# Optimization experiments

Hardware: AMD Instinct MI355X
Metric: run time of the kernel (lower is better)

## Reference

```python
import jax, jax.numpy as jnp
import numpy as np

B, N, F_IN = 8, 4096, 32
NRP = 1024
D_MODEL = 512
K = 64  # max_num_neighbors
STAGE_CFG = ((1024, 0.05), (256, 0.3), (64, 0.5))  # (num_samples=ceil(0.25*N_in), radius)


def fps(pos, m):
    """Farthest point sampling of m points from pos (N,3), deterministic start at 0."""
    d = jnp.sum((pos - pos[0]) ** 2, axis=-1)
    idxs = jnp.zeros((m,), jnp.int32)
    def body(i, carry):
        idxs, d = carry
        nxt = jnp.argmax(d).astype(jnp.int32)
        d = jnp.minimum(d, jnp.sum((pos - pos[nxt]) ** 2, axis=-1))
        return (idxs.at[i].set(nxt), d)
    idxs, _ = jax.lax.fori_loop(1, m, body, (idxs, d))
    return idxs


def apply_mlp(h, ws, bs):
    for w, b in zip(ws[:-1], bs[:-1]):
        h = jax.nn.relu(h @ w + b)
    return h @ ws[-1] + bs[-1]


def sa_stage(x, pos, m, r, ws, bs):
    """SAModule: FPS -> radius neighbors (<=K) -> PointNetConv (gather, MLP, max-scatter)."""
    idx = jax.vmap(lambda p: fps(p, m))(pos)                          # (B,m)
    pos_s = jnp.take_along_axis(pos, idx[..., None], axis=1)          # (B,m,3)
    d2 = jnp.sum((pos_s[:, :, None, :] - pos[:, None, :, :]) ** 2, -1)  # (B,m,N)
    neg = jnp.where(d2 <= r * r, -d2, -jnp.inf)
    vals, nbr = jax.lax.top_k(neg, K)                                 # (B,m,K) nearest within r
    valid = vals > -jnp.inf                                           # self always valid (d2=0)
    x_j = jax.vmap(lambda xb, nb: xb[nb])(x, nbr)                     # (B,m,K,F) gather
    p_j = jax.vmap(lambda pb, nb: pb[nb])(pos, nbr)                   # (B,m,K,3)
    h = jnp.concatenate([x_j, p_j - pos_s[:, :, None, :]], axis=-1)   # message input
    h = apply_mlp(h, ws, bs)
    h = jnp.where(valid[..., None], h, -jnp.inf)
    return jnp.max(h, axis=2), pos_s                                  # max aggregation


def _forward(point_cloud_features, point_cloud, emb_table, point_id_emb, stage_params):
    x = emb_table[point_cloud_features[..., 0]]                       # (B,N,F_IN)
    x = x.at[:, :NRP].add(point_id_emb)
    pos = point_cloud
    for (m, r), (ws, bs) in zip(STAGE_CFG, stage_params):
        x, pos = sa_stage(x, pos, m, r, ws, bs)
    return x, pos                                                     # (B,64,D_MODEL), (B,64,3)


def setup_inputs() -> dict:
    key = jax.random.key(0)
    ks = iter(jax.random.split(key, 64))
    def nrm(shape, s=0.05):
        return s * jax.random.normal(next(ks), shape, dtype=jnp.float32)
    inp = {
        "point_cloud_features": jax.random.randint(next(ks), (B, N, 1), 0, 3),
        "point_cloud": jax.random.uniform(next(ks), (B, N, 3), dtype=jnp.float32),
        "emb_table": nrm((3, F_IN), 1.0),
        "point_id_emb": nrm((1, NRP, F_IN), 1.0),
    }
    dims = {"s1": [3 + F_IN, 64, 64, 64], "s2": [64 + 3, 128, 128, 256], "s3": [256 + 3, 256, 512, D_MODEL]}
    for s, d in dims.items():
        for i in range(3):
            inp[f"{s}w{i}"] = nrm((d[i], d[i + 1]))
            inp[f"{s}b{i}"] = jnp.zeros((d[i + 1],), jnp.float32)
    return inp


def reference(point_cloud_features, point_cloud, emb_table, point_id_emb,
              s1w0, s1b0, s1w1, s1b1, s1w2, s1b2,
              s2w0, s2b0, s2w1, s2b1, s2w2, s2b2,
              s3w0, s3b0, s3w1, s3b1, s3w2, s3b2):
    stage_params = [
        ([s1w0, s1w1, s1w2], [s1b0, s1b1, s1b2]),
        ([s2w0, s2w1, s2w2], [s2b0, s2b1, s2b2]),
        ([s3w0, s3w1, s3w2], [s3b0, s3b1, s3b2]),
    ]
    return _forward(point_cloud_features, point_cloud, emb_table, point_id_emb, stage_params)
```

## Files before the change

### kernel.cpp

```cpp
#include <hip/hip_runtime.h>

#define DEVI static __device__ __forceinline__

constexpr int B = 8;
constexpr int N0 = 4096;
constexpr int KNB = 64;

typedef float f32x2 __attribute__((ext_vector_type(2)));

DEVI float dist2f(float ax, float ay, float az, float bx, float by, float bz) {
#pragma clang fp contract(off)
  float dx = ax - bx;
  float dy = ay - by;
  float dz = az - bz;
  return (dx * dx + dy * dy) + dz * dz;
}
DEVI f32x2 dist2v(f32x2 ax, f32x2 ay, f32x2 az, float bx, float by, float bz) {
#pragma clang fp contract(off)
  f32x2 dx = ax - bx;
  f32x2 dy = ay - by;
  f32x2 dz = az - bz;
  return (dx * dx + dy * dy) + dz * dz;
}

DEVI unsigned long long packMinKey(float v, int i) {
  return ((unsigned long long)__float_as_uint(v) << 32) | (unsigned int)i;
}

template <int CTRL, int RM>
DEVI float dppMaxF32(float v) {
  int o = __builtin_amdgcn_update_dpp(__float_as_int(v), __float_as_int(v),
                                      CTRL, RM, 0xf, false);
  return fmaxf(v, __int_as_float(o));
}
DEVI float waveMaxF32(float v) {
  v = dppMaxF32<0x111, 0xf>(v);
  v = dppMaxF32<0x112, 0xf>(v);
  v = dppMaxF32<0x114, 0xf>(v);
  v = dppMaxF32<0x118, 0xf>(v);
  v = dppMaxF32<0x142, 0xa>(v);
  v = dppMaxF32<0x143, 0xc>(v);
  return __int_as_float(__builtin_amdgcn_readlane(__float_as_int(v), 63));
}
template <int CTRL, int RM>
DEVI unsigned dppMinU32(unsigned v) {
  int o = __builtin_amdgcn_update_dpp((int)v, (int)v, CTRL, RM, 0xf, false);
  unsigned ov = (unsigned)o;
  return v < ov ? v : ov;
}
DEVI unsigned waveMinU32(unsigned v) {
  v = dppMinU32<0x111, 0xf>(v);
  v = dppMinU32<0x112, 0xf>(v);
  v = dppMinU32<0x114, 0xf>(v);
  v = dppMinU32<0x118, 0xf>(v);
  v = dppMinU32<0x142, 0xa>(v);
  v = dppMinU32<0x143, 0xc>(v);
  return (unsigned)__builtin_amdgcn_readlane((int)v, 63);
}

__global__ void __launch_bounds__(256) x0_kernel(const int* __restrict__ feat,
                                                 const float* __restrict__ emb,
                                                 const float* __restrict__ pid,
                                                 float* __restrict__ x0) {
  int gid = blockIdx.x * 256 + threadIdx.x;
  if (gid >= B * N0 * 32) return;
  int c = gid & 31;
  int bn = gid >> 5;
  int n = bn & (N0 - 1);
  int f = feat[bn];
  float v = emb[f * 32 + c];
  if (n < 1024) v += pid[n * 32 + c];
  x0[gid] = v;
}

template <int NPTS, int M, int BLK>
__global__ void __launch_bounds__(BLK) fps_kernel(const float* __restrict__ pos,
                                                  float* __restrict__ pos_out) {
  constexpr int EPT = NPTS / BLK;
  constexpr int EP2 = EPT / 2;
  constexpr int NW = BLK / 64;
  __shared__ float4 posl[NPTS];
  __shared__ float4 outp[M];
  __shared__ alignas(16) unsigned long long redk[2][NW < 2 ? 2 : NW];
  const int b = blockIdx.x;
  const int t = threadIdx.x;
  const float* pb = pos + (size_t)b * NPTS * 3;
  f32x2 px[EP2], py[EP2], pz[EP2], d[EP2];
#pragma unroll
  for (int e = 0; e < EP2; ++e) {
    int i0 = t + (2 * e) * BLK;
    int i1 = t + (2 * e + 1) * BLK;
    float x0 = pb[i0 * 3 + 0], y0 = pb[i0 * 3 + 1], z0 = pb[i0 * 3 + 2];
    float x1 = pb[i1 * 3 + 0], y1 = pb[i1 * 3 + 1], z1 = pb[i1 * 3 + 2];
    px[e] = (f32x2){x0, x1};
    py[e] = (f32x2){y0, y1};
    pz[e] = (f32x2){z0, z1};
    posl[i0] = make_float4(x0, y0, z0, 0.f);
    posl[i1] = make_float4(x1, y1, z1, 0.f);
  }
  float sx = pb[0], sy = pb[1], sz = pb[2];
  if (t == 0) outp[0] = make_float4(sx, sy, sz, 0.f);
#pragma unroll
  for (int e = 0; e < EP2; ++e) d[e] = dist2v(px[e], py[e], pz[e], sx, sy, sz);

  for (int it = 1; it < M; ++it) {
    float lm = fmaxf(d[0].x, d[0].y);
#pragma unroll
    for (int e = 1; e < EP2; ++e) lm = fmaxf(lm, fmaxf(d[e].x, d[e].y));
    const float vstar = waveMaxF32(lm);
    unsigned cand = 0xffffffffu;
#pragma unroll
    for (int e = 0; e < EP2; ++e) {
      unsigned c0 = (d[e].x == vstar) ? (unsigned)(t + (2 * e) * BLK) : 0xffffffffu;
      unsigned c1 = (d[e].y == vstar) ? (unsigned)(t + (2 * e + 1) * BLK) : 0xffffffffu;
      cand = cand < c0 ? cand : c0;
      cand = cand < c1 ? cand : c1;
    }
    cand = waveMinU32(cand);
    unsigned sel;
    if constexpr (NW > 1) {
      if ((t & 63) == 0) {
        unsigned long long key =
            ((unsigned long long)__float_as_uint(vstar) << 32) |
            (unsigned)(0x7fffffffu - cand);
        redk[it & 1][t >> 6] = key;
      }
      __syncthreads();
      unsigned long long kk = redk[it & 1][0];
#pragma unroll
      for (int w = 1; w < NW; ++w) {
        unsigned long long o = redk[it & 1][w];
        kk = (kk > o) ? kk : o;
      }
      sel = 0x7fffffffu - (unsigned)(kk & 0xffffffffULL);
    } else {
      sel = cand;
    }
    float4 sp = posl[sel];
    if (t == 0) outp[it] = sp;
#pragma unroll
    for (int e = 0; e < EP2; ++e) {
      f32x2 nd = dist2v(px[e], py[e], pz[e], sp.x, sp.y, sp.z);
      d[e].x = fminf(d[e].x, nd.x);
      d[e].y = fminf(d[e].y, nd.y);
    }
  }
  __syncthreads();
  for (int m = t; m < M; m += BLK) {
    float4 q = outp[m];
    pos_out[(size_t)(b * M + m) * 3 + 0] = q.x;
    pos_out[(size_t)(b * M + m) * 3 + 1] = q.y;
    pos_out[(size_t)(b * M + m) * 3 + 2] = q.z;
  }
}

template <int NPTS, int M>
__global__ void __launch_bounds__(256) radius_kernel(const float* __restrict__ pos,
                                                     const float* __restrict__ pos_s,
                                                     float r2,
                                                     int* __restrict__ nbr,
                                                     int* __restrict__ cnt) {
  __shared__ unsigned long long candkey[NPTS];
  __shared__ int ctr;
  const int blk = blockIdx.x;
  const int t = threadIdx.x;
  const int b = blk / M;
  const float* pb = pos + (size_t)b * NPTS * 3;
  const float cx = pos_s[(size_t)blk * 3 + 0];
  const float cy = pos_s[(size_t)blk * 3 + 1];
  const float cz = pos_s[(size_t)blk * 3 + 2];
  if (t == 0) ctr = 0;
  __syncthreads();
  for (int j = t; j < NPTS; j += 256) {
    float d2 = dist2f(pb[j * 3 + 0], pb[j * 3 + 1], pb[j * 3 + 2], cx, cy, cz);
    if (d2 <= r2) {
      int p = atomicAdd(&ctr, 1);
      candkey[p] = packMinKey(d2, j);
      if (p < KNB) nbr[(size_t)blk * KNB + p] = j;
    }
  }
  __syncthreads();
  const int c = ctr;
  if (c <= KNB) {
    if (t == 0) cnt[blk] = c;
    return;
  }
  for (int s = t; s < c; s += 256) {
    unsigned long long mykey = candkey[s];
    int rank = 0;
#pragma unroll 4
    for (int j = 0; j < c; ++j) {
      rank += (candkey[j] < mykey) ? 1 : 0;
    }
    if (rank < KNB)
      nbr[(size_t)blk * KNB + rank] = (int)(unsigned)(mykey & 0xffffffffULL);
  }
  if (t == 0) cnt[blk] = KNB;
}

__global__ void __launch_bounds__(64) conv1_kernel(
    const float* __restrict__ x0, const float* __restrict__ pos,
    const float* __restrict__ pos_s, const int* __restrict__ nbr,
    const int* __restrict__ cntp,
    const float* __restrict__ w0, const float* __restrict__ b0,
    const float* __restrict__ w1, const float* __restrict__ b1,
    const float* __restrict__ w2, const float* __restrict__ b2,
    float* __restrict__ x1) {
  __shared__ float ins[35];
  __shared__ float h[64];
  const int blk = blockIdx.x;
  const int t = threadIdx.x;
  const int b = blk >> 10;
  const int c = cntp[blk];
  const float cx = pos_s[(size_t)blk * 3 + 0];
  const float cy = pos_s[(size_t)blk * 3 + 1];
  const float cz = pos_s[(size_t)blk * 3 + 2];
  float best = -__builtin_inff();
  for (int r = 0; r < c; ++r) {
    int j = nbr[(size_t)blk * KNB + r];
    if (t < 32) {
      ins[t] = x0[((size_t)(b * N0) + j) * 32 + t];
    } else if (t < 35) {
      float pv = pos[((size_t)(b * N0) + j) * 3 + (t - 32)];
      float cv = (t == 32) ? cx : (t == 33) ? cy : cz;
      ins[t] = pv - cv;
    }
    __syncthreads();
    float v = b0[t];
#pragma unroll
    for (int i = 0; i < 35; ++i) v = fmaf(ins[i], w0[i * 64 + t], v);
    v = fmaxf(v, 0.f);
    h[t] = v;
    __syncthreads();
    float v2 = b1[t];
#pragma unroll
    for (int i = 0; i < 64; ++i) v2 = fmaf(h[i], w1[i * 64 + t], v2);
    v2 = fmaxf(v2, 0.f);
    __syncthreads();
    h[t] = v2;
    __syncthreads();
    float v3 = b2[t];
#pragma unroll
    for (int i = 0; i < 64; ++i) v3 = fmaf(h[i], w2[i * 64 + t], v3);
    best = fmaxf(best, v3);
    __syncthreads();
  }
  x1[(size_t)blk * 64 + t] = best;
}

__global__ void __launch_bounds__(256) conv2_kernel(
    const float* __restrict__ x1, const float* __restrict__ pos1,
    const float* __restrict__ pos2, const int* __restrict__ nbr,
    const int* __restrict__ cntp,
    const float* __restrict__ w0, const float* __restrict__ b0,
    const float* __restrict__ w1, const float* __restrict__ b1,
    const float* __restrict__ w2, const float* __restrict__ b2,
    float* __restrict__ x2) {
  __shared__ __attribute__((aligned(16))) float msg[64][68];
  __shared__ __attribute__((aligned(16))) float h[64][128];
  __shared__ float red[8][256];
  const int blk = blockIdx.x;
  const int t = threadIdx.x;
  const int b = blk >> 8;
  const int c = cntp[blk];
  const float cx = pos2[(size_t)blk * 3 + 0];
  const float cy = pos2[(size_t)blk * 3 + 1];
  const float cz = pos2[(size_t)blk * 3 + 2];
  for (int idx = t; idx < 64 * 68; idx += 256) {
    int r = idx / 68;
    int k = idx - r * 68;
    float v = 0.f;
    if (r < c && k < 67) {
      int j = nbr[(size_t)blk * KNB + r];
      if (k < 64) {
        v = x1[((size_t)(b * 1024) + j) * 64 + k];
      } else {
        float pv = pos1[((size_t)(b * 1024) + j) * 3 + (k - 64)];
        v = pv - ((k == 64) ? cx : (k == 65) ? cy : cz);
      }
    }
    msg[r][k] = v;
  }
  __syncthreads();
  const int rg = t >> 5;
  const int cg = t & 31;
  {
    float acc[8][4] = {};
    for (int i4 = 0; i4 < 16; ++i4) {
      float wv[4][4];
#pragma unroll
      for (int k = 0; k < 4; ++k) {
        float4 q = *(const float4*)&w0[(size_t)(i4 * 4 + k) * 128 + cg * 4];
        wv[k][0] = q.x; wv[k][1] = q.y; wv[k][2] = q.z; wv[k][3] = q.w;
      }
#pragma unroll
      for (int rr = 0; rr < 8; ++rr) {
        float4 aq = *(const float4*)&msg[rg * 8 + rr][i4 * 4];
        float a[4] = {aq.x, aq.y, aq.z, aq.w};
#pragma unroll
        for (int k = 0; k < 4; ++k)
#pragma unroll
          for (int cc = 0; cc < 4; ++cc)
            acc[rr][cc] = fmaf(a[k], wv[k][cc], acc[rr][cc]);
      }
    }
#pragma unroll
    for (int i = 64; i < 67; ++i) {
      float wv[4];
#pragma unroll
      for (int cc = 0; cc < 4; ++cc) wv[cc] = w0[(size_t)i * 128 + cg * 4 + cc];
#pragma unroll
      for (int rr = 0; rr < 8; ++rr) {
        float a = msg[rg * 8 + rr][i];
#pragma unroll
        for (int cc = 0; cc < 4; ++cc) acc[rr][cc] = fmaf(a, wv[cc], acc[rr][cc]);
      }
    }
#pragma unroll
    for (int rr = 0; rr < 8; ++rr)
#pragma unroll
      for (int cc = 0; cc < 4; ++cc)
        h[rg * 8 + rr][cg * 4 + cc] = fmaxf(acc[rr][cc] + b0[cg * 4 + cc], 0.f);
  }
  __syncthreads();
  {
    float acc[8][4] = {};
    for (int i4 = 0; i4 < 32; ++i4) {
      float wv[4][4];
#pragma unroll
      for (int k = 0; k < 4; ++k) {
        float4 q = *(const float4*)&w1[(size_t)(i4 * 4 + k) * 128 + cg * 4];
        wv[k][0] = q.x; wv[k][1] = q.y; wv[k][2] = q.z; wv[k][3] = q.w;
      }
#pragma unroll
      for (int rr = 0; rr < 8; ++rr) {
        float4 aq = *(const float4*)&h[rg * 8 + rr][i4 * 4];
        float a[4] = {aq.x, aq.y, aq.z, aq.w};
#pragma unroll
        for (int k = 0; k < 4; ++k)
#pragma unroll
          for (int cc = 0; cc < 4; ++cc)
            acc[rr][cc] = fmaf(a[k], wv[k][cc], acc[rr][cc]);
      }
    }
    __syncthreads();
#pragma unroll
    for (int rr = 0; rr < 8; ++rr)
#pragma unroll
      for (int cc = 0; cc < 4; ++cc)
        h[rg * 8 + rr][cg * 4 + cc] = fmaxf(acc[rr][cc] + b1[cg * 4 + cc], 0.f);
  }
  __syncthreads();
  {
    float acc[8][8] = {};
    for (int i4 = 0; i4 < 32; ++i4) {
      float wv[4][8];
#pragma unroll
      for (int k = 0; k < 4; ++k) {
        float4 q0 = *(const float4*)&w2[(size_t)(i4 * 4 + k) * 256 + cg * 8];
        float4 q1 = *(const float4*)&w2[(size_t)(i4 * 4 + k) * 256 + cg * 8 + 4];
        wv[k][0] = q0.x; wv[k][1] = q0.y; wv[k][2] = q0.z; wv[k][3] = q0.w;
        wv[k][4] = q1.x; wv[k][5] = q1.y; wv[k][6] = q1.z; wv[k][7] = q1.w;
      }
#pragma unroll
      for (int rr = 0; rr < 8; ++rr) {
        float4 aq = *(const float4*)&h[rg * 8 + rr][i4 * 4];
        float a[4] = {aq.x, aq.y, aq.z, aq.w};
#pragma unroll
        for (int k = 0; k < 4; ++k)
#pragma unroll
          for (int cc = 0; cc < 8; ++cc)
            acc[rr][cc] = fmaf(a[k], wv[k][cc], acc[rr][cc]);
      }
    }
    float mx[8];
#pragma unroll
    for (int cc = 0; cc < 8; ++cc) mx[cc] = -__builtin_inff();
#pragma unroll
    for (int rr = 0; rr < 8; ++rr) {
      if (rg * 8 + rr < c) {
#pragma unroll
        for (int cc = 0; cc < 8; ++cc)
          mx[cc] = fmaxf(mx[cc], acc[rr][cc] + b2[cg * 8 + cc]);
      }
    }
#pragma unroll
    for (int cc = 0; cc < 8; ++cc) red[rg][cg * 8 + cc] = mx[cc];
  }
  __syncthreads();
  {
    float v = red[0][t];
#pragma unroll
    for (int g = 1; g < 8; ++g) v = fmaxf(v, red[g][t]);
    x2[(size_t)blk * 256 + t] = v;
  }
}

__global__ void __launch_bounds__(256) conv3_kernel(
    const float* __restrict__ x2, const float* __restrict__ pos2,
    const float* __restrict__ pos3, const int* __restrict__ nbr,
    const int* __restrict__ cntp,
    const float* __restrict__ w0, const float* __restrict__ b0,
    const float* __restrict__ w1, const float* __restrict__ b1,
    const float* __restrict__ w2, const float* __restrict__ b2,
    float* __restrict__ out) {
  __shared__ __attribute__((aligned(16))) float msg[16][260];
  __shared__ __attribute__((aligned(16))) float h[16][512];
  __shared__ float red[4][512];
  __shared__ float omax[512];
  const int blk = blockIdx.x;
  const int t = threadIdx.x;
  const int b = blk >> 6;
  const int c = cntp[blk];
  const float cx = pos3[(size_t)blk * 3 + 0];
  const float cy = pos3[(size_t)blk * 3 + 1];
  const float cz = pos3[(size_t)blk * 3 + 2];
  omax[t] = -__builtin_inff();
  omax[t + 256] = -__builtin_inff();
  const int rg = t >> 6;
  const int cg = t & 63;
  __syncthreads();
  for (int ch = 0; ch < 4; ++ch) {
    if (ch * 16 >= c) break;
    for (int idx = t; idx < 16 * 260; idx += 256) {
      int r = idx / 260;
      int k = idx - r * 260;
      int rglob = ch * 16 + r;
      float v = 0.f;
      if (rglob < c && k < 259) {
        int j = nbr[(size_t)blk * KNB + rglob];
        if (k < 256) {
          v = x2[((size_t)(b * 256) + j) * 256 + k];
        } else {
          float pv = pos2[((size_t)(b * 256) + j) * 3 + (k - 256)];
          v = pv - ((k == 256) ? cx : (k == 257) ? cy : cz);
        }
      }
      msg[r][k] = v;
    }
    __syncthreads();
    {
      float acc[4][4] = {};
      for (int i4 = 0; i4 < 64; ++i4) {
        float wv[4][4];
#pragma unroll
        for (int k = 0; k < 4; ++k) {
          float4 q = *(const float4*)&w0[(size_t)(i4 * 4 + k) * 256 + cg * 4];
          wv[k][0] = q.x; wv[k][1] = q.y; wv[k][2] = q.z; wv[k][3] = q.w;
        }
#pragma unroll
        for (int rr = 0; rr < 4; ++rr) {
          float4 aq = *(const float4*)&msg[rg * 4 + rr][i4 * 4];
          float a[4] = {aq.x, aq.y, aq.z, aq.w};
#pragma unroll
          for (int k = 0; k < 4; ++k)
#pragma unroll
            for (int cc = 0; cc < 4; ++cc)
              acc[rr][cc] = fmaf(a[k], wv[k][cc], acc[rr][cc]);
        }
      }
#pragma unroll
      for (int i = 256; i < 259; ++i) {
        float wv[4];
#pragma unroll
        for (int cc = 0; cc < 4; ++cc) wv[cc] = w0[(size_t)i * 256 + cg * 4 + cc];
#pragma unroll
        for (int rr = 0; rr < 4; ++rr) {
          float a = msg[rg * 4 + rr][i];
#pragma unroll
          for (int cc = 0; cc < 4; ++cc) acc[rr][cc] = fmaf(a, wv[cc], acc[rr][cc]);
        }
      }
#pragma unroll
      for (int rr = 0; rr < 4; ++rr)
#pragma unroll
        for (int cc = 0; cc < 4; ++cc)
          h[rg * 4 + rr][cg * 4 + cc] = fmaxf(acc[rr][cc] + b0[cg * 4 + cc], 0.f);
    }
    __syncthreads();
    {
      float acc[4][8] = {};
      for (int i4 = 0; i4 < 64; ++i4) {
        float wv[4][8];
#pragma unroll
        for (int k = 0; k < 4; ++k) {
          float4 q0 = *(const float4*)&w1[(size_t)(i4 * 4 + k) * 512 + cg * 8];
          float4 q1 = *(const float4*)&w1[(size_t)(i4 * 4 + k) * 512 + cg * 8 + 4];
          wv[k][0] = q0.x; wv[k][1] = q0.y; wv[k][2] = q0.z; wv[k][3] = q0.w;
          wv[k][4] = q1.x; wv[k][5] = q1.y; wv[k][6] = q1.z; wv[k][7] = q1.w;
        }
#pragma unroll
        for (int rr = 0; rr < 4; ++rr) {
          float4 aq = *(const float4*)&h[rg * 4 + rr][i4 * 4];
          float a[4] = {aq.x, aq.y, aq.z, aq.w};
#pragma unroll
          for (int k = 0; k < 4; ++k)
#pragma unroll
            for (int cc = 0; cc < 8; ++cc)
              acc[rr][cc] = fmaf(a[k], wv[k][cc], acc[rr][cc]);
        }
      }
      __syncthreads();
#pragma unroll
      for (int rr = 0; rr < 4; ++rr)
#pragma unroll
        for (int cc = 0; cc < 8; ++cc)
          h[rg * 4 + rr][cg * 8 + cc] = fmaxf(acc[rr][cc] + b1[cg * 8 + cc], 0.f);
    }
    __syncthreads();
    {
      float acc[4][8] = {};
      for (int i4 = 0; i4 < 128; ++i4) {
        float wv[4][8];
#pragma unroll
        for (int k = 0; k < 4; ++k) {
          float4 q0 = *(const float4*)&w2[(size_t)(i4 * 4 + k) * 512 + cg * 8];
          float4 q1 = *(const float4*)&w2[(size_t)(i4 * 4 + k) * 512 + cg * 8 + 4];
          wv[k][0] = q0.x; wv[k][1] = q0.y; wv[k][2] = q0.z; wv[k][3] = q0.w;
          wv[k][4] = q1.x; wv[k][5] = q1.y; wv[k][6] = q1.z; wv[k][7] = q1.w;
        }
#pragma unroll
        for (int rr = 0; rr < 4; ++rr) {
          float4 aq = *(const float4*)&h[rg * 4 + rr][i4 * 4];
          float a[4] = {aq.x, aq.y, aq.z, aq.w};
#pragma unroll
          for (int k = 0; k < 4; ++k)
#pragma unroll
            for (int cc = 0; cc < 8; ++cc)
              acc[rr][cc] = fmaf(a[k], wv[k][cc], acc[rr][cc]);
        }
      }
      float mx[8];
#pragma unroll
      for (int cc = 0; cc < 8; ++cc) mx[cc] = -__builtin_inff();
#pragma unroll
      for (int rr = 0; rr < 4; ++rr) {
        if (ch * 16 + rg * 4 + rr < c) {
#pragma unroll
          for (int cc = 0; cc < 8; ++cc)
            mx[cc] = fmaxf(mx[cc], acc[rr][cc] + b2[cg * 8 + cc]);
        }
      }
#pragma unroll
      for (int cc = 0; cc < 8; ++cc) red[rg][cg * 8 + cc] = mx[cc];
    }
    __syncthreads();
    for (int k = t; k < 512; k += 256) {
      float v = omax[k];
#pragma unroll
      for (int g = 0; g < 4; ++g) v = fmaxf(v, red[g][k]);
      omax[k] = v;
    }
    __syncthreads();
  }
  out[(size_t)blk * 512 + t] = omax[t];
  out[(size_t)blk * 512 + t + 256] = omax[t + 256];
}

extern "C" void kernel_launch(void* const* d_in, const int* in_sizes, int n_in,
                              void* d_out, int out_size, void* d_ws, size_t ws_size,
                              hipStream_t stream) {
  const int* feat = (const int*)d_in[0];
  const float* pos = (const float*)d_in[1];
  const float* emb = (const float*)d_in[2];
  const float* pid = (const float*)d_in[3];
  const float* s1w0 = (const float*)d_in[4];
  const float* s1b0 = (const float*)d_in[5];
  const float* s1w1 = (const float*)d_in[6];
  const float* s1b1 = (const float*)d_in[7];
  const float* s1w2 = (const float*)d_in[8];
  const float* s1b2 = (const float*)d_in[9];
  const float* s2w0 = (const float*)d_in[10];
  const float* s2b0 = (const float*)d_in[11];
  const float* s2w1 = (const float*)d_in[12];
  const float* s2b1 = (const float*)d_in[13];
  const float* s2w2 = (const float*)d_in[14];
  const float* s2b2 = (const float*)d_in[15];
  const float* s3w0 = (const float*)d_in[16];
  const float* s3b0 = (const float*)d_in[17];
  const float* s3w1 = (const float*)d_in[18];
  const float* s3b1 = (const float*)d_in[19];
  const float* s3w2 = (const float*)d_in[20];
  const float* s3b2 = (const float*)d_in[21];
  (void)in_sizes; (void)n_in; (void)out_size; (void)ws_size;

  char* ws = (char*)d_ws;
  size_t off = 0;
  auto alloc = [&](size_t nbytes) {
    void* p = ws + off;
    off = (off + nbytes + 255) & ~(size_t)255;
    return p;
  };
  float* x0 = (float*)alloc((size_t)B * N0 * 32 * 4);
  float* pos1 = (float*)alloc((size_t)B * 1024 * 3 * 4);
  int* nbr1 = (int*)alloc((size_t)B * 1024 * KNB * 4);
  int* cnt1 = (int*)alloc((size_t)B * 1024 * 4);
  float* x1 = (float*)alloc((size_t)B * 1024 * 64 * 4);
  float* pos2 = (float*)alloc((size_t)B * 256 * 3 * 4);
  int* nbr2 = (int*)alloc((size_t)B * 256 * KNB * 4);
  int* cnt2 = (int*)alloc((size_t)B * 256 * 4);
  float* x2 = (float*)alloc((size_t)B * 256 * 256 * 4);
  int* nbr3 = (int*)alloc((size_t)B * 64 * KNB * 4);
  int* cnt3 = (int*)alloc((size_t)B * 64 * 4);

  float* xout = (float*)d_out;
  float* pos3 = xout + (size_t)B * 64 * 512;

  const float r2a = (float)(0.05 * 0.05);
  const float r2b = (float)(0.3 * 0.3);
  const float r2c = (float)(0.5 * 0.5);

  x0_kernel<<<(B * N0 * 32 + 255) / 256, 256, 0, stream>>>(feat, emb, pid, x0);

  fps_kernel<4096, 1024, 256><<<B, 256, 0, stream>>>(pos, pos1);
  radius_kernel<4096, 1024><<<B * 1024, 256, 0, stream>>>(pos, pos1, r2a, nbr1, cnt1);
  conv1_kernel<<<B * 1024, 64, 0, stream>>>(x0, pos, pos1, nbr1, cnt1,
                                            s1w0, s1b0, s1w1, s1b1, s1w2, s1b2, x1);

  fps_kernel<1024, 256, 256><<<B, 256, 0, stream>>>(pos1, pos2);
  radius_kernel<1024, 256><<<B * 256, 256, 0, stream>>>(pos1, pos2, r2b, nbr2, cnt2);
  conv2_kernel<<<B * 256, 256, 0, stream>>>(x1, pos1, pos2, nbr2, cnt2,
                                            s2w0, s2b0, s2w1, s2b1, s2w2, s2b2, x2);

  fps_kernel<256, 64, 64><<<B, 64, 0, stream>>>(pos2, pos3);
  radius_kernel<256, 64><<<B * 64, 256, 0, stream>>>(pos2, pos3, r2c, nbr3, cnt3);
  conv3_kernel<<<B * 64, 256, 0, stream>>>(x2, pos2, pos3, nbr3, cnt3,
                                           s3w0, s3b0, s3w1, s3b1, s3w2, s3b2, xout);
}
```

Baseline: 1.543 ms.

## Fuse independent pipeline stages into shared launches to overlap FPS with radius/conv

Turns the stage kernels into device functions and merges independent work into four combined launches, dispatched by block index. Each level's serial FPS now runs alongside the previous level's x0 build, radius search or conv, instead of in its own 8-block launch. conv1 now handles four neighbours per 256-thread block, and FPS tracks its running max inside the distance-update loop rather than in a separate pass. The cost is one shared-memory size per merged kernel, so light blocks (such as the x0 ones in l1) reserve more LDS than they use, which may reduce occupancy.

```diff
diff --git a/kernel.cpp b/kernel.cpp
--- a/kernel.cpp
+++ b/kernel.cpp
@@ -58,11 +58,11 @@
   return (unsigned)__builtin_amdgcn_readlane((int)v, 63);
 }
 
-__global__ void __launch_bounds__(256) x0_kernel(const int* __restrict__ feat,
-                                                 const float* __restrict__ emb,
-                                                 const float* __restrict__ pid,
-                                                 float* __restrict__ x0) {
-  int gid = blockIdx.x * 256 + threadIdx.x;
+
+DEVI void x0_body(const int* __restrict__ feat, const float* __restrict__ emb,
+                  const float* __restrict__ pid, float* __restrict__ x0buf,
+                  int bx, int t) {
+  int gid = bx * 256 + t;
   if (gid >= B * N0 * 32) return;
   int c = gid & 31;
   int bn = gid >> 5;
@@ -70,20 +70,19 @@
   int f = feat[bn];
   float v = emb[f * 32 + c];
   if (n < 1024) v += pid[n * 32 + c];
-  x0[gid] = v;
+  x0buf[gid] = v;
 }
 
 template <int NPTS, int M, int BLK>
-__global__ void __launch_bounds__(BLK) fps_kernel(const float* __restrict__ pos,
-                                                  float* __restrict__ pos_out) {
+DEVI void fps_body(char* smem, const float* __restrict__ pos,
+                   float* __restrict__ pos_out, int b, int t) {
   constexpr int EPT = NPTS / BLK;
   constexpr int EP2 = EPT / 2;
   constexpr int NW = BLK / 64;
-  __shared__ float4 posl[NPTS];
-  __shared__ float4 outp[M];
-  __shared__ alignas(16) unsigned long long redk[2][NW < 2 ? 2 : NW];
-  const int b = blockIdx.x;
-  const int t = threadIdx.x;
+  float4* posl = (float4*)smem;
+  float4* outp = (float4*)(smem + (size_t)NPTS * 16);
+  unsigned long long* redk =
+      (unsigned long long*)(smem + (size_t)(NPTS + M) * 16);
   const float* pb = pos + (size_t)b * NPTS * 3;
   f32x2 px[EP2], py[EP2], pz[EP2], d[EP2];
 #pragma unroll
@@ -100,14 +99,15 @@
   }
   float sx = pb[0], sy = pb[1], sz = pb[2];
   if (t == 0) outp[0] = make_float4(sx, sy, sz, 0.f);
-#pragma unroll
-  for (int e = 0; e < EP2; ++e) d[e] = dist2v(px[e], py[e], pz[e], sx, sy, sz);
-
+  f32x2 m2 = (f32x2){-1.f, -1.f};
+#pragma unroll
+  for (int e = 0; e < EP2; ++e) {
+    d[e] = dist2v(px[e], py[e], pz[e], sx, sy, sz);
+    m2.x = fmaxf(m2.x, d[e].x);
+    m2.y = fmaxf(m2.y, d[e].y);
+  }
   for (int it = 1; it < M; ++it) {
-    float lm = fmaxf(d[0].x, d[0].y);
-#pragma unroll
-    for (int e = 1; e < EP2; ++e) lm = fmaxf(lm, fmaxf(d[e].x, d[e].y));
-    const float vstar = waveMaxF32(lm);
+    const float vstar = waveMaxF32(fmaxf(m2.x, m2.y));
     unsigned cand = 0xffffffffu;
 #pragma unroll
     for (int e = 0; e < EP2; ++e) {
@@ -123,13 +123,13 @@
         unsigned long long key =
             ((unsigned long long)__float_as_uint(vstar) << 32) |
             (unsigned)(0x7fffffffu - cand);
-        redk[it & 1][t >> 6] = key;
+        redk[(it & 1) * NW + (t >> 6)] = key;
       }
       __syncthreads();
-      unsigned long long kk = redk[it & 1][0];
+      unsigned long long kk = redk[(it & 1) * NW + 0];
 #pragma unroll
       for (int w = 1; w < NW; ++w) {
-        unsigned long long o = redk[it & 1][w];
+        unsigned long long o = redk[(it & 1) * NW + w];
         kk = (kk > o) ? kk : o;
       }
       sel = 0x7fffffffu - (unsigned)(kk & 0xffffffffULL);
@@ -138,14 +138,17 @@
     }
     float4 sp = posl[sel];
     if (t == 0) outp[it] = sp;
+    m2 = (f32x2){-1.f, -1.f};
 #pragma unroll
     for (int e = 0; e < EP2; ++e) {
       f32x2 nd = dist2v(px[e], py[e], pz[e], sp.x, sp.y, sp.z);
       d[e].x = fminf(d[e].x, nd.x);
       d[e].y = fminf(d[e].y, nd.y);
-    }
-  }
-  __syncthreads();
+      m2.x = fmaxf(m2.x, d[e].x);
+      m2.y = fmaxf(m2.y, d[e].y);
+    }
+  }
+  if constexpr (NW > 1) __syncthreads();
   for (int m = t; m < M; m += BLK) {
     float4 q = outp[m];
     pos_out[(size_t)(b * M + m) * 3 + 0] = q.x;
@@ -155,32 +158,29 @@
 }
 
 template <int NPTS, int M>
-__global__ void __launch_bounds__(256) radius_kernel(const float* __restrict__ pos,
-                                                     const float* __restrict__ pos_s,
-                                                     float r2,
-                                                     int* __restrict__ nbr,
-                                                     int* __restrict__ cnt) {
-  __shared__ unsigned long long candkey[NPTS];
-  __shared__ int ctr;
-  const int blk = blockIdx.x;
-  const int t = threadIdx.x;
+DEVI void radius_body(char* smem, const float* __restrict__ pos,
+                      const float* __restrict__ pos_s, float r2,
+                      int* __restrict__ nbr, int* __restrict__ cnt, int blk,
+                      int t) {
+  unsigned long long* candkey = (unsigned long long*)smem;
+  int* ctrp = (int*)(smem + (size_t)NPTS * 8);
   const int b = blk / M;
   const float* pb = pos + (size_t)b * NPTS * 3;
   const float cx = pos_s[(size_t)blk * 3 + 0];
   const float cy = pos_s[(size_t)blk * 3 + 1];
   const float cz = pos_s[(size_t)blk * 3 + 2];
-  if (t == 0) ctr = 0;
+  if (t == 0) *ctrp = 0;
   __syncthreads();
   for (int j = t; j < NPTS; j += 256) {
     float d2 = dist2f(pb[j * 3 + 0], pb[j * 3 + 1], pb[j * 3 + 2], cx, cy, cz);
     if (d2 <= r2) {
-      int p = atomicAdd(&ctr, 1);
+      int p = atomicAdd(ctrp, 1);
       candkey[p] = packMinKey(d2, j);
       if (p < KNB) nbr[(size_t)blk * KNB + p] = j;
     }
   }
   __syncthreads();
-  const int c = ctr;
+  const int c = *ctrp;
   if (c <= KNB) {
     if (t == 0) cnt[blk] = c;
     return;
@@ -198,69 +198,77 @@
   if (t == 0) cnt[blk] = KNB;
 }
 
-__global__ void __launch_bounds__(64) conv1_kernel(
-    const float* __restrict__ x0, const float* __restrict__ pos,
-    const float* __restrict__ pos_s, const int* __restrict__ nbr,
-    const int* __restrict__ cntp,
-    const float* __restrict__ w0, const float* __restrict__ b0,
-    const float* __restrict__ w1, const float* __restrict__ b1,
-    const float* __restrict__ w2, const float* __restrict__ b2,
-    float* __restrict__ x1) {
-  __shared__ float ins[35];
-  __shared__ float h[64];
-  const int blk = blockIdx.x;
-  const int t = threadIdx.x;
+DEVI void conv1_body(char* smem, const float* __restrict__ x0buf,
+                     const float* __restrict__ pos,
+                     const float* __restrict__ pos_s,
+                     const int* __restrict__ nbr, const int* __restrict__ cntp,
+                     const float* __restrict__ w0, const float* __restrict__ b0,
+                     const float* __restrict__ w1, const float* __restrict__ b1,
+                     const float* __restrict__ w2, const float* __restrict__ b2,
+                     float* __restrict__ x1, int blk, int t) {
+  float(*ins)[36] = (float(*)[36])smem;
+  float(*hh)[65] = (float(*)[65])(smem + 576);
+  float(*sred)[65] = (float(*)[65])(smem + 1616);
+  const int slot = t >> 6;
+  const int ch = t & 63;
   const int b = blk >> 10;
   const int c = cntp[blk];
   const float cx = pos_s[(size_t)blk * 3 + 0];
   const float cy = pos_s[(size_t)blk * 3 + 1];
   const float cz = pos_s[(size_t)blk * 3 + 2];
   float best = -__builtin_inff();
-  for (int r = 0; r < c; ++r) {
-    int j = nbr[(size_t)blk * KNB + r];
-    if (t < 32) {
-      ins[t] = x0[((size_t)(b * N0) + j) * 32 + t];
-    } else if (t < 35) {
-      float pv = pos[((size_t)(b * N0) + j) * 3 + (t - 32)];
-      float cv = (t == 32) ? cx : (t == 33) ? cy : cz;
-      ins[t] = pv - cv;
-    }
-    __syncthreads();
-    float v = b0[t];
-#pragma unroll
-    for (int i = 0; i < 35; ++i) v = fmaf(ins[i], w0[i * 64 + t], v);
+  for (int r0 = 0; r0 < c; r0 += 4) {
+    const int r = r0 + slot;
+    const bool act = r < c;
+    const int j = nbr[(size_t)blk * KNB + (act ? r : 0)];
+    if (ch < 32) {
+      ins[slot][ch] = x0buf[((size_t)(b * N0) + j) * 32 + ch];
+    } else if (ch < 35) {
+      float pv = pos[((size_t)(b * N0) + j) * 3 + (ch - 32)];
+      float cv = (ch == 32) ? cx : (ch == 33) ? cy : cz;
+      ins[slot][ch] = pv - cv;
+    }
+    __syncthreads();
+    float v = b0[ch];
+#pragma unroll
+    for (int i = 0; i < 35; ++i) v = fmaf(ins[slot][i], w0[i * 64 + ch], v);
     v = fmaxf(v, 0.f);
-    h[t] = v;
-    __syncthreads();
-    float v2 = b1[t];
-#pragma unroll
-    for (int i = 0; i < 64; ++i) v2 = fmaf(h[i], w1[i * 64 + t], v2);
+    hh[slot][ch] = v;
+    __syncthreads();
+    float v2 = b1[ch];
+#pragma unroll
+    for (int i = 0; i < 64; ++i) v2 = fmaf(hh[slot][i], w1[i * 64 + ch], v2);
     v2 = fmaxf(v2, 0.f);
     __syncthreads();
-    h[t] = v2;
-    __syncthreads();
-    float v3 = b2[t];
-#pragma unroll
-    for (int i = 0; i < 64; ++i) v3 = fmaf(h[i], w2[i * 64 + t], v3);
-    best = fmaxf(best, v3);
-    __syncthreads();
-  }
-  x1[(size_t)blk * 64 + t] = best;
-}
-
-__global__ void __launch_bounds__(256) conv2_kernel(
-    const float* __restrict__ x1, const float* __restrict__ pos1,
-    const float* __restrict__ pos2, const int* __restrict__ nbr,
-    const int* __restrict__ cntp,
-    const float* __restrict__ w0, const float* __restrict__ b0,
-    const float* __restrict__ w1, const float* __restrict__ b1,
-    const float* __restrict__ w2, const float* __restrict__ b2,
-    float* __restrict__ x2) {
-  __shared__ __attribute__((aligned(16))) float msg[64][68];
-  __shared__ __attribute__((aligned(16))) float h[64][128];
-  __shared__ float red[8][256];
-  const int blk = blockIdx.x;
-  const int t = threadIdx.x;
+    hh[slot][ch] = v2;
+    __syncthreads();
+    float v3 = b2[ch];
+#pragma unroll
+    for (int i = 0; i < 64; ++i) v3 = fmaf(hh[slot][i], w2[i * 64 + ch], v3);
+    if (act) best = fmaxf(best, v3);
+    __syncthreads();
+  }
+  sred[slot][ch] = best;
+  __syncthreads();
+  if (t < 64) {
+    float v = sred[0][t];
+#pragma unroll
+    for (int s = 1; s < 4; ++s) v = fmaxf(v, sred[s][t]);
+    x1[(size_t)blk * 64 + t] = v;
+  }
+}
+
+DEVI void conv2_body(char* smem, const float* __restrict__ x1,
+                     const float* __restrict__ pos1,
+                     const float* __restrict__ pos2,
+                     const int* __restrict__ nbr, const int* __restrict__ cntp,
+                     const float* __restrict__ w0, const float* __restrict__ b0,
+                     const float* __restrict__ w1, const float* __restrict__ b1,
+                     const float* __restrict__ w2, const float* __restrict__ b2,
+                     float* __restrict__ x2, int blk, int t) {
+  float(*msg)[68] = (float(*)[68])smem;
+  float(*h)[128] = (float(*)[128])(smem + 17408);
+  float(*red)[256] = (float(*)[256])(smem + 17408 + 32768);
   const int b = blk >> 8;
   const int c = cntp[blk];
   const float cx = pos2[(size_t)blk * 3 + 0];
@@ -393,6 +401,73 @@
 #pragma unroll
     for (int g = 1; g < 8; ++g) v = fmaxf(v, red[g][t]);
     x2[(size_t)blk * 256 + t] = v;
+  }
+}
+
+
+__global__ void __launch_bounds__(256) l1_kernel(
+    const float* __restrict__ pos, float* __restrict__ pos1,
+    const int* __restrict__ feat, const float* __restrict__ emb,
+    const float* __restrict__ pid, float* __restrict__ x0buf) {
+  __shared__ __attribute__((aligned(16))) char smem[81984];
+  if (blockIdx.x < 8) {
+    fps_body<4096, 1024, 256>(smem, pos, pos1, blockIdx.x, threadIdx.x);
+  } else {
+    x0_body(feat, emb, pid, x0buf, blockIdx.x - 8, threadIdx.x);
+  }
+}
+
+__global__ void __launch_bounds__(256) l2_kernel(
+    const float* __restrict__ pos1, float* __restrict__ pos2,
+    const float* __restrict__ pos, float r2a, int* __restrict__ nbr1,
+    int* __restrict__ cnt1) {
+  __shared__ __attribute__((aligned(16))) char smem[33024];
+  if (blockIdx.x < 8) {
+    fps_body<1024, 256, 256>(smem, pos1, pos2, blockIdx.x, threadIdx.x);
+  } else {
+    radius_body<4096, 1024>(smem, pos, pos1, r2a, nbr1, cnt1, blockIdx.x - 8,
+                            threadIdx.x);
+  }
+}
+
+__global__ void __launch_bounds__(256) l3_kernel(
+    const float* __restrict__ pos2, float* __restrict__ pos3, float r2b,
+    int* __restrict__ nbr2, int* __restrict__ cnt2,
+    const float* __restrict__ pos1, const float* __restrict__ x0buf,
+    const float* __restrict__ pos, const int* __restrict__ nbr1,
+    const int* __restrict__ cnt1, const float* __restrict__ w0,
+    const float* __restrict__ b0, const float* __restrict__ w1,
+    const float* __restrict__ b1, const float* __restrict__ w2,
+    const float* __restrict__ b2, float* __restrict__ x1) {
+  __shared__ __attribute__((aligned(16))) char smem[8448];
+  if (blockIdx.x < 8) {
+    if (threadIdx.x < 64)
+      fps_body<256, 64, 64>(smem, pos2, pos3, blockIdx.x, threadIdx.x);
+  } else if (blockIdx.x < 8 + 2048) {
+    radius_body<1024, 256>(smem, pos1, pos2, r2b, nbr2, cnt2, blockIdx.x - 8,
+                           threadIdx.x);
+  } else {
+    conv1_body(smem, x0buf, pos, pos1, nbr1, cnt1, w0, b0, w1, b1, w2, b2, x1,
+               blockIdx.x - (8 + 2048), threadIdx.x);
+  }
+}
+
+__global__ void __launch_bounds__(256) l4_kernel(
+    const float* __restrict__ pos2, const float* __restrict__ pos3, float r2c,
+    int* __restrict__ nbr3, int* __restrict__ cnt3,
+    const float* __restrict__ x1, const float* __restrict__ pos1,
+    const int* __restrict__ nbr2, const int* __restrict__ cnt2,
+    const float* __restrict__ w0, const float* __restrict__ b0,
+    const float* __restrict__ w1, const float* __restrict__ b1,
+    const float* __restrict__ w2, const float* __restrict__ b2,
+    float* __restrict__ x2) {
+  __shared__ __attribute__((aligned(16))) char smem[58368];
+  if (blockIdx.x < 512) {
+    radius_body<256, 64>(smem, pos2, pos3, r2c, nbr3, cnt3, blockIdx.x,
+                         threadIdx.x);
+  } else {
+    conv2_body(smem, x1, pos1, pos2, nbr2, cnt2, w0, b0, w1, b1, w2, b2, x2,
+               blockIdx.x - 512, threadIdx.x);
   }
 }
 
@@ -610,20 +685,14 @@
   const float r2b = (float)(0.3 * 0.3);
   const float r2c = (float)(0.5 * 0.5);
 
-  x0_kernel<<<(B * N0 * 32 + 255) / 256, 256, 0, stream>>>(feat, emb, pid, x0);
-
-  fps_kernel<4096, 1024, 256><<<B, 256, 0, stream>>>(pos, pos1);
-  radius_kernel<4096, 1024><<<B * 1024, 256, 0, stream>>>(pos, pos1, r2a, nbr1, cnt1);
-  conv1_kernel<<<B * 1024, 64, 0, stream>>>(x0, pos, pos1, nbr1, cnt1,
-                                            s1w0, s1b0, s1w1, s1b1, s1w2, s1b2, x1);
-
-  fps_kernel<1024, 256, 256><<<B, 256, 0, stream>>>(pos1, pos2);
-  radius_kernel<1024, 256><<<B * 256, 256, 0, stream>>>(pos1, pos2, r2b, nbr2, cnt2);
-  conv2_kernel<<<B * 256, 256, 0, stream>>>(x1, pos1, pos2, nbr2, cnt2,
-                                            s2w0, s2b0, s2w1, s2b1, s2w2, s2b2, x2);
-
-  fps_kernel<256, 64, 64><<<B, 64, 0, stream>>>(pos2, pos3);
-  radius_kernel<256, 64><<<B * 64, 256, 0, stream>>>(pos2, pos3, r2c, nbr3, cnt3);
+  l1_kernel<<<8 + 4096, 256, 0, stream>>>(pos, pos1, feat, emb, pid, x0);
+  l2_kernel<<<8 + 8192, 256, 0, stream>>>(pos1, pos2, pos, r2a, nbr1, cnt1);
+  l3_kernel<<<8 + 2048 + 8192, 256, 0, stream>>>(
+      pos2, pos3, r2b, nbr2, cnt2, pos1, x0, pos, nbr1, cnt1,
+      s1w0, s1b0, s1w1, s1b1, s1w2, s1b2, x1);
+  l4_kernel<<<512 + 2048, 256, 0, stream>>>(
+      pos2, pos3, r2c, nbr3, cnt3, x1, pos1, nbr2, cnt2,
+      s2w0, s2b0, s2w1, s2b1, s2w2, s2b2, x2);
   conv3_kernel<<<B * 64, 256, 0, stream>>>(x2, pos2, pos3, nbr3, cnt3,
                                            s3w0, s3b0, s3w1, s3b1, s3w2, s3b2, xout);
 }
```

After: 1.517 ms. About the same (-1.7%).
